# Optimization experiments

Measured on AMD Instinct MI355X. Metric: run time of the kernel, lower is better.

The kernel has to match this reference:

```python
import jax, jax.numpy as jnp
import numpy as np

B, NPG, DEG = 32, 1024, 16          # graphs, nodes/graph, avg degree
N, E = B * NPG, B * NPG * DEG        # 32768 nodes, 524288 edges
IN_C, HID, H, EDGE_D = 128, 64, 4, 8
RATIO = 0.5
K = int(np.ceil(RATIO * NPG))        # 512 nodes kept per graph (static)
SLOPE = 0.2                          # PyG GATConv LeakyReLU default


def setup_inputs() -> dict:
    key = jax.random.key(0)
    ks = jax.random.split(key, 10)
    x = jax.random.normal(ks[0], (N, IN_C), jnp.float32)
    # edges confined within each graph (block structure like PyG Batch)
    src_l = jax.random.randint(ks[1], (B, NPG * DEG), 0, NPG)
    dst_l = jax.random.randint(ks[2], (B, NPG * DEG), 0, NPG)
    off = (jnp.arange(B) * NPG)[:, None]
    edge_index = jnp.stack([(src_l + off).reshape(-1), (dst_l + off).reshape(-1)]).astype(jnp.int64)
    edge = jax.random.normal(ks[3], (E, EDGE_D), jnp.float32)
    batch_index = jnp.repeat(jnp.arange(B), NPG).astype(jnp.int64)
    s_in = 1.0 / np.sqrt(IN_C)
    W = jax.random.normal(ks[4], (IN_C, H, HID), jnp.float32) * s_in
    a_src = jax.random.normal(ks[5], (H, HID), jnp.float32) * s_in
    a_dst = jax.random.normal(ks[6], (H, HID), jnp.float32) * s_in
    b_gat = jnp.zeros((H * HID,), jnp.float32)
    W_lin = jax.random.normal(ks[7], (H * HID, HID), jnp.float32) * (1.0 / np.sqrt(H * HID))
    b_lin = jnp.zeros((HID,), jnp.float32)
    p_pool = jax.random.normal(ks[8], (HID,), jnp.float32)
    return dict(x=x, edge_index=edge_index, edge=edge, batch_index=batch_index,
                W=W, a_src=a_src, a_dst=a_dst, b_gat=b_gat,
                W_lin=W_lin, b_lin=b_lin, p_pool=p_pool)


def reference(x, edge_index, edge, batch_index, W, a_src, a_dst, b_gat, W_lin, b_lin, p_pool):
    n = x.shape[0]
    # --- GATConv (heads concat, self-loops added, softmax over incoming edges) ---
    loops = jnp.arange(n)
    src = jnp.concatenate([edge_index[0], loops])
    dst = jnp.concatenate([edge_index[1], loops])
    h = jnp.einsum('ni,ihc->nhc', x, W)                  # [N,H,C]
    al_src = (h * a_src).sum(-1)                          # [N,H]
    al_dst = (h * a_dst).sum(-1)                          # [N,H]
    e = jax.nn.leaky_relu(al_src[src] + al_dst[dst], SLOPE)  # [Etot,H]
    m = jax.ops.segment_max(e, dst, num_segments=n)
    ex = jnp.exp(e - m[dst])
    denom = jax.ops.segment_sum(ex, dst, num_segments=n)
    alpha = ex / denom[dst]                               # segment softmax per target
    out = jax.ops.segment_sum(h[src] * alpha[:, :, None], dst, num_segments=n)
    xg = out.reshape(n, H * HID) + b_gat
    # --- Linear ---
    xl = xg @ W_lin + b_lin                               # [N,HID]
    # --- TopKPooling (tanh(x.p/||p||) score, top ceil(ratio*n) per graph) ---
    score = jnp.tanh(xl @ p_pool / jnp.linalg.norm(p_pool))   # [N]
    topv, topi = jax.lax.top_k(score.reshape(B, NPG), K)      # [B,K]
    perm = (topi + (jnp.arange(B) * NPG)[:, None]).reshape(-1)  # global kept node ids
    xp = xl[perm] * topv.reshape(-1)[:, None]             # [B*K,HID], gated by score
    batch_out = jnp.repeat(jnp.arange(B), K)
    # edge filtering / remapping (padded with -1 instead of compacting)
    nmap = jnp.full((n,), -1, jnp.int32).at[perm].set(jnp.arange(B * K, dtype=jnp.int32))
    ns, nd = nmap[edge_index[0]], nmap[edge_index[1]]
    valid = (ns >= 0) & (nd >= 0)
    edge_index_new = jnp.where(valid, jnp.stack([ns, nd]), -1)
    edge_new = jnp.where(valid[:, None], edge, 0.0)
    # --- global mean/max pool (graphs are contiguous blocks of K nodes) ---
    xr = xp.reshape(B, K, HID)
    x1 = jnp.concatenate([xr.mean(axis=1), xr.max(axis=1)], axis=-1)  # [B,2*HID]
    return xp, edge_index_new, edge_new, batch_out, x1
```

## Files before the change

kernel.cpp:

```cpp
#include <hip/hip_runtime.h>
#include <math.h>

#define NN   32768
#define EE   524288
#define ETOT (EE + NN)
#define BB   32
#define NPG  1024
#define EPG  16384
#define RPG  17408
#define KK   512
#define INC  128
#define HID  64
#define NH   4
#define CC   256
#define SLOPE 0.2f

typedef __attribute__((ext_vector_type(8))) short short8;
typedef __attribute__((ext_vector_type(4))) float f32x4;

static __device__ inline unsigned short f2bf(float f) {
  unsigned u = __float_as_uint(f);
  unsigned r = (u + 0x7FFFu + ((u >> 16) & 1u)) >> 16;
  return (unsigned short)r;
}

__global__ __launch_bounds__(256) void prep_kernel(const float* __restrict__ W,
                                                   const float* __restrict__ a_src,
                                                   const float* __restrict__ a_dst,
                                                   const float* __restrict__ b_gat,
                                                   const float* __restrict__ W_lin,
                                                   const float* __restrict__ b_lin,
                                                   const float* __restrict__ p,
                                                   float* __restrict__ Mg,
                                                   float* __restrict__ cbuf,
                                                   unsigned short* __restrict__ Wt,
                                                   unsigned short* __restrict__ Wlt) {
  const int b = blockIdx.x, t = threadIdx.x;
  if (b >= 17) {
    int idx = (b - 17) * 256 + t;
    if (idx < 32768) {
      int c = idx >> 7, k = idx & 127;
      Wt[idx] = f2bf(W[k * 256 + c]);
    } else {
      int i2 = idx - 32768;
      int c = i2 >> 8, k = i2 & 255;
      Wlt[i2] = f2bf(W_lin[k * 64 + c]);
    }
    return;
  }
  __shared__ float pl[64];
  __shared__ float ql[256];
  __shared__ float red[256];
  __shared__ float red2[256];
  if (t < 64) pl[t] = p[t];
  __syncthreads();
  {
    float acc = 0.f;
    const float* wr = W_lin + t * 64;
#pragma unroll
    for (int c = 0; c < 64; c += 4) {
      float4 wv = *(const float4*)(wr + c);
      acc += wv.x * pl[c] + wv.y * pl[c + 1] + wv.z * pl[c + 2] + wv.w * pl[c + 3];
    }
    ql[t] = acc;
  }
  __syncthreads();
  if (b == 0) {
    float r = ql[t] * b_gat[t];
    if (t < 64) r += b_lin[t] * pl[t];
    red[t] = r;
    red2[t] = (t < 64) ? pl[t] * pl[t] : 0.f;
    __syncthreads();
    for (int s2 = 128; s2 > 0; s2 >>= 1) {
      if (t < s2) { red[t] += red[t + s2]; red2[t] += red2[t + s2]; }
      __syncthreads();
    }
    if (t == 0) { cbuf[0] = red[0]; cbuf[1] = 1.0f / sqrtf(red2[0]); }
    return;
  }
  if (t < 96) {
    const int i = (b - 1) * 8 + t / 12;
    const int j = t % 12;
    const int hh = j & 3;
    const float* wr = W + i * 256 + hh * 64;
    float acc = 0.f;
    if (j < 8) {
      const float* v = (j < 4 ? a_src : a_dst) + hh * 64;
#pragma unroll
      for (int c = 0; c < 64; c += 4) {
        float4 wv = *(const float4*)(wr + c);
        float4 vv = *(const float4*)(v + c);
        acc += wv.x * vv.x + wv.y * vv.y + wv.z * vv.z + wv.w * vv.w;
      }
    } else {
#pragma unroll
      for (int c = 0; c < 64; ++c) acc += wr[c] * ql[hh * 64 + c];
    }
    Mg[i * 12 + j] = acc;
  }
}

__global__ __launch_bounds__(256) void stage2_kernel(const float* __restrict__ x,
                                                     const float* __restrict__ Mg,
                                                     const unsigned short* __restrict__ Wt,
                                                     float* __restrict__ al_s,
                                                     float* __restrict__ al_d,
                                                     float* __restrict__ hq,
                                                     unsigned short* __restrict__ hbf) {
  __shared__ float smem[76 * 132];
  const int t = threadIdx.x;
  if (blockIdx.x >= 512) {
    float (*xs)[132] = (float(*)[132])smem;
    float (*MsT)[132] = (float(*)[132])(smem + 64 * 132);
    const int n0 = (blockIdx.x - 512) * 64;
    for (int r = t; r < 1536; r += 256) MsT[r % 12][r / 12] = Mg[r];
#pragma unroll
    for (int u = 0; u < 8; ++u) {
      int idx = u * 256 + t;
      int node = idx >> 5, c4 = idx & 31;
      *(float4*)(&xs[node][c4 * 4]) =
          *(const float4*)(x + (size_t)(n0 + node) * 128 + c4 * 4);
    }
    __syncthreads();
    const int node = t >> 2, q = t & 3;
    const int j0 = q * 3;
    float a0 = 0.f, a1 = 0.f, a2 = 0.f;
#pragma unroll
    for (int c4 = 0; c4 < 32; ++c4) {
      float4 xv = *(const float4*)(&xs[node][c4 * 4]);
      float4 m0 = *(const float4*)(&MsT[j0 + 0][c4 * 4]);
      float4 m1 = *(const float4*)(&MsT[j0 + 1][c4 * 4]);
      float4 m2 = *(const float4*)(&MsT[j0 + 2][c4 * 4]);
      a0 += xv.x * m0.x + xv.y * m0.y + xv.z * m0.z + xv.w * m0.w;
      a1 += xv.x * m1.x + xv.y * m1.y + xv.z * m1.z + xv.w * m1.w;
      a2 += xv.x * m2.x + xv.y * m2.y + xv.z * m2.z + xv.w * m2.w;
    }
    const int n = n0 + node;
    float vals[3] = {a0, a1, a2};
#pragma unroll
    for (int k = 0; k < 3; ++k) {
      int j = j0 + k;
      float* base = (j < 4) ? al_s : ((j < 8) ? al_d : hq);
      int jj = (j < 4) ? j : ((j < 8) ? j - 4 : j - 8);
      base[n * 4 + jj] = vals[k];
    }
    return;
  }
  const int lane = t & 63;
  const int wv = t >> 6;
  const int q = lane >> 4, nh = lane & 15;
  const int lid = blockIdx.x;
  const int node = ((lid & 7) * 64 + (lid >> 3)) * 64 + wv * 16 + nh;
  f32x4 acc[16];
#pragma unroll
  for (int mt = 0; mt < 16; ++mt) acc[mt] = (f32x4){0.f, 0.f, 0.f, 0.f};
  const float* xr = x + (size_t)node * 128;
#pragma unroll
  for (int kc = 0; kc < 4; ++kc) {
    const float* xp = xr + kc * 32 + q * 8;
    float4 v0 = *(const float4*)(xp);
    float4 v1 = *(const float4*)(xp + 4);
    short8 b;
    b[0] = (short)f2bf(v0.x); b[1] = (short)f2bf(v0.y);
    b[2] = (short)f2bf(v0.z); b[3] = (short)f2bf(v0.w);
    b[4] = (short)f2bf(v1.x); b[5] = (short)f2bf(v1.y);
    b[6] = (short)f2bf(v1.z); b[7] = (short)f2bf(v1.w);
#pragma unroll
    for (int mt = 0; mt < 16; ++mt) {
      short8 a = *(const short8*)(Wt + (size_t)(mt * 16 + nh) * 128 + kc * 32 + q * 8);
      acc[mt] = __builtin_amdgcn_mfma_f32_16x16x32_bf16(a, b, acc[mt], 0, 0, 0);
    }
  }
  unsigned short* hr = hbf + (size_t)node * 256;
#pragma unroll
  for (int mt = 0; mt < 16; ++mt) {
    ushort4 o;
    o.x = f2bf(acc[mt][0]); o.y = f2bf(acc[mt][1]);
    o.z = f2bf(acc[mt][2]); o.w = f2bf(acc[mt][3]);
    *(ushort4*)(hr + mt * 16 + q * 4) = o;
  }
}

__global__ __launch_bounds__(1024) void scan_scatter_kernel(const int* __restrict__ ei,
                                                            int* __restrict__ row_ptr,
                                                            int* __restrict__ col) {
  __shared__ int hist[NPG];
  __shared__ int lpos[NPG];
  __shared__ int wsum[16];
  const int b = blockIdx.x, t = threadIdx.x;
  const int lane = t & 63, wid = t >> 6;
  hist[t] = 0;
  __syncthreads();
  const int e0 = b * EPG;
  for (int k = t; k < EPG; k += 1024)
    atomicAdd(&hist[ei[EE + e0 + k] - b * NPG], 1);
  __syncthreads();
  const int c = hist[t] + 1;
  int inc = c;
#pragma unroll
  for (int off = 1; off < 64; off <<= 1) {
    int u = __shfl_up(inc, off, 64);
    if (lane >= off) inc += u;
  }
  if (lane == 63) wsum[wid] = inc;
  __syncthreads();
  if (wid == 0) {
    int v = (lane < 16) ? wsum[lane] : 0;
#pragma unroll
    for (int off = 1; off < 16; off <<= 1) {
      int u = __shfl_up(v, off, 64);
      if (lane >= off) v += u;
    }
    if (lane < 16) wsum[lane] = v;
  }
  __syncthreads();
  const int woff = (wid == 0) ? 0 : wsum[wid - 1];
  const int excl = woff + inc - c;
  row_ptr[b * NPG + t] = b * RPG + excl;
  lpos[t] = excl;
  if (b == 0 && t == 0) row_ptr[NN] = ETOT;
  __syncthreads();
  {
    int p0 = atomicAdd(&lpos[t], 1);
    col[b * RPG + p0] = b * NPG + t;
  }
  for (int k = t; k < EPG; k += 1024) {
    int s = ei[e0 + k];
    int d = ei[EE + e0 + k];
    int p1 = atomicAdd(&lpos[d - b * NPG], 1);
    col[b * RPG + p1] = s;
  }
}

__global__ __launch_bounds__(256) void agg_kernel(const unsigned short* __restrict__ h,
                                                  const float* __restrict__ al_s,
                                                  const float* __restrict__ al_d,
                                                  const float* __restrict__ hq,
                                                  const int* __restrict__ row_ptr,
                                                  const int* __restrict__ col,
                                                  const float* __restrict__ b_gat,
                                                  const float* __restrict__ cbuf,
                                                  unsigned short* __restrict__ outg,
                                                  float* __restrict__ score) {
  __shared__ float wsh[4][256];
  __shared__ float qsh[4][256];
  __shared__ int   osh[4][64];
  const int lane = threadIdx.x & 63;
  const int wv = threadIdx.x >> 6;
  const int hqi = lane >> 4;
  const int xcd = blockIdx.x & 7;
  const int jb = blockIdx.x >> 3;
  const int n = (xcd * 1024 + jb) * 4 + wv;
  const int beg = row_ptr[n], end = row_ptr[n + 1];
  const float4 ad4 = *(const float4*)(al_d + (size_t)n * 4);
  const char* hbase = (const char*)h + (size_t)lane * 8;
  float ax = 0.f, ay = 0.f, az = 0.f, aw = 0.f, den = 0.f, sq = 0.f;
  for (int base = beg; base < end; base += 64) {
    const int rem = end - base;
    const int cnt = rem < 64 ? rem : 64;
    if (lane < cnt) {
      const int c = col[base + lane];
      osh[wv][lane] = c << 9;
      const float4 as = *(const float4*)(al_s + (size_t)c * 4);
      float e0 = as.x + ad4.x; e0 = (e0 > 0.f) ? e0 : SLOPE * e0;
      float e1 = as.y + ad4.y; e1 = (e1 > 0.f) ? e1 : SLOPE * e1;
      float e2 = as.z + ad4.z; e2 = (e2 > 0.f) ? e2 : SLOPE * e2;
      float e3 = as.w + ad4.w; e3 = (e3 > 0.f) ? e3 : SLOPE * e3;
      *(float4*)(&wsh[wv][lane * 4]) =
          make_float4(__expf(e0), __expf(e1), __expf(e2), __expf(e3));
      *(float4*)(&qsh[wv][lane * 4]) = *(const float4*)(hq + (size_t)c * 4);
    }
    const int cm1 = cnt - 1;
    uint2 v0 = *(const uint2*)(hbase + osh[wv][0]);
    uint2 v1 = *(const uint2*)(hbase + osh[wv][1 > cm1 ? cm1 : 1]);
    uint2 v2 = *(const uint2*)(hbase + osh[wv][2 > cm1 ? cm1 : 2]);
    uint2 v3 = *(const uint2*)(hbase + osh[wv][3 > cm1 ? cm1 : 3]);
    for (int i = 0; i < cnt; ++i) {
      const float w = wsh[wv][i * 4 + hqi];
      const float hqv = qsh[wv][i * 4 + hqi];
      uint2 cur = v0; v0 = v1; v1 = v2; v2 = v3;
      int ni = i + 4; ni = ni > cm1 ? cm1 : ni;
      v3 = *(const uint2*)(hbase + osh[wv][ni]);
      den += w; sq += w * hqv;
      ax += w * __uint_as_float(cur.x << 16);
      ay += w * __uint_as_float(cur.x & 0xffff0000u);
      az += w * __uint_as_float(cur.y << 16);
      aw += w * __uint_as_float(cur.y & 0xffff0000u);
    }
  }
  const float4 bg = *(const float4*)(b_gat + lane * 4);
  ushort4 ov;
  ov.x = f2bf(ax / den + bg.x); ov.y = f2bf(ay / den + bg.y);
  ov.z = f2bf(az / den + bg.z); ov.w = f2bf(aw / den + bg.w);
  *(ushort4*)(outg + (size_t)n * 256 + lane * 4) = ov;
  float sd = sq / den;
  float s0v = __shfl(sd, 0), s1v = __shfl(sd, 16);
  float s2v = __shfl(sd, 32), s3v = __shfl(sd, 48);
  if (lane == 0)
    score[n] = tanhf((s0v + s1v + s2v + s3v + cbuf[0]) * cbuf[1]);
}

__global__ __launch_bounds__(1024) void topk_kernel(const float* __restrict__ score,
                                                    int* __restrict__ pidx_g,
                                                    float* __restrict__ tvs_g,
                                                    int* __restrict__ nmap,
                                                    float* __restrict__ out_batch) {
  __shared__ float scv[NPG];
  const int blk = blockIdx.x;
  const int b = blk >> 3, slice = blk & 7;
  const int t = threadIdx.x;
  scv[t] = score[b * NPG + t];
  __syncthreads();
  const int node = slice * 128 + (t >> 3);
  const int sub = t & 7;
  const float sc = scv[node];
  int rank = 0;
#pragma unroll
  for (int m = 0; m < 32; ++m) {
    const int j = (m * 8 + sub) * 4;
    const float4 s4 = *(const float4*)(&scv[j]);
    rank += (s4.x > sc) || (s4.x == sc && (j + 0) < node);
    rank += (s4.y > sc) || (s4.y == sc && (j + 1) < node);
    rank += (s4.z > sc) || (s4.z == sc && (j + 2) < node);
    rank += (s4.w > sc) || (s4.w == sc && (j + 3) < node);
  }
  rank += __shfl_xor(rank, 1, 64);
  rank += __shfl_xor(rank, 2, 64);
  rank += __shfl_xor(rank, 4, 64);
  if (sub == 0) {
    const int gn = b * NPG + node;
    if (rank < KK) {
      pidx_g[b * KK + rank] = node;
      tvs_g[b * KK + rank] = sc;
      nmap[gn] = b * KK + rank;
      out_batch[b * KK + rank] = (float)b;
    } else {
      nmap[gn] = -1;
    }
  }
}

__global__ __launch_bounds__(256) void gemm2xp_kernel(const unsigned short* __restrict__ outg,
                                                      const unsigned short* __restrict__ Wlt,
                                                      const float* __restrict__ bl,
                                                      const int* __restrict__ pidx_g,
                                                      const float* __restrict__ tvs_g,
                                                      float* __restrict__ out_xp,
                                                      float* __restrict__ psum,
                                                      float* __restrict__ pmax) {
  __shared__ float tile[64][68];
  __shared__ float pr[4][64];
  __shared__ float pmx[4][64];
  const int t = threadIdx.x;
  const int lane = t & 63, wv = t >> 6;
  const int q = lane >> 4, nh = lane & 15;
  const int g = blockIdx.x >> 3, o = blockIdx.x & 7;
  const int r = o * 64 + wv * 16 + nh;
  const int row = wv * 16 + nh;
  const int gnode = g * NPG + pidx_g[g * KK + r];
  const float tv = tvs_g[g * KK + r];
  f32x4 acc[4];
#pragma unroll
  for (int mt = 0; mt < 4; ++mt) acc[mt] = (f32x4){0.f, 0.f, 0.f, 0.f};
  const unsigned short* ar = outg + (size_t)gnode * 256;
#pragma unroll
  for (int kc = 0; kc < 8; ++kc) {
    short8 bf = *(const short8*)(ar + kc * 32 + q * 8);
#pragma unroll
    for (int mt = 0; mt < 4; ++mt) {
      short8 a = *(const short8*)(Wlt + (size_t)(mt * 16 + nh) * 256 + kc * 32 + q * 8);
      acc[mt] = __builtin_amdgcn_mfma_f32_16x16x32_bf16(a, bf, acc[mt], 0, 0, 0);
    }
  }
#pragma unroll
  for (int mt = 0; mt < 4; ++mt) {
    const int c4 = mt * 16 + q * 4;
    float4 bl4 = *(const float4*)(bl + c4);
    float4 o4 = make_float4((acc[mt][0] + bl4.x) * tv, (acc[mt][1] + bl4.y) * tv,
                            (acc[mt][2] + bl4.z) * tv, (acc[mt][3] + bl4.w) * tv);
    *(float4*)(out_xp + (size_t)(g * KK + r) * HID + c4) = o4;
    *(float4*)(&tile[row][c4]) = o4;
  }
  __syncthreads();
  {
    const int ch = t & 63, qr = t >> 6;
    float s = 0.f, m = -INFINITY;
#pragma unroll
    for (int rr = 0; rr < 16; ++rr) {
      float v = tile[qr * 16 + rr][ch];
      s += v; m = fmaxf(m, v);
    }
    pr[qr][ch] = s; pmx[qr][ch] = m;
  }
  __syncthreads();
  if (t < 64) {
    float s = pr[0][t] + pr[1][t] + pr[2][t] + pr[3][t];
    float m = fmaxf(fmaxf(pr[0][t], pr[1][t]), fmaxf(pr[2][t], pr[3][t]));
    m = fmaxf(fmaxf(pmx[0][t], pmx[1][t]), fmaxf(pmx[2][t], pmx[3][t]));
    psum[g * 512 + o * 64 + t] = s;
    pmax[g * 512 + o * 64 + t] = m;
  }
}

__global__ void edge_out_kernel(const int* __restrict__ ei, const float* __restrict__ edge,
                                const int* __restrict__ nmap,
                                const float* __restrict__ psum,
                                const float* __restrict__ pmax,
                                float* __restrict__ out_ei, float* __restrict__ out_edge,
                                float* __restrict__ out_x1) {
  if (blockIdx.x < BB && threadIdx.x < 64) {
    const int b = blockIdx.x, t = threadIdx.x;
    float s = 0.f, m = -INFINITY;
#pragma unroll
    for (int o = 0; o < 8; ++o) {
      s += psum[b * 512 + o * 64 + t];
      m = fmaxf(m, pmax[b * 512 + o * 64 + t]);
    }
    out_x1[b * 128 + t] = s * (1.0f / KK);
    out_x1[b * 128 + 64 + t] = m;
  }
  int e = blockIdx.x * 256 + threadIdx.x;
  if (e >= EE) return;
  int s = ei[e], d = ei[EE + e];
  int ns = nmap[s], nd = nmap[d];
  bool valid = (ns >= 0) && (nd >= 0);
  out_ei[e] = (float)(valid ? ns : -1);
  out_ei[EE + e] = (float)(valid ? nd : -1);
  const float4* ef = (const float4*)(edge + (size_t)e * 8);
  float4 z = make_float4(0.f, 0.f, 0.f, 0.f);
  float4 v0 = valid ? ef[0] : z;
  float4 v1 = valid ? ef[1] : z;
  float4* eo = (float4*)(out_edge + (size_t)e * 8);
  eo[0] = v0; eo[1] = v1;
}

extern "C" void kernel_launch(void* const* d_in, const int* in_sizes, int n_in,
                              void* d_out, int out_size, void* d_ws, size_t ws_size,
                              hipStream_t stream) {
  const float* x      = (const float*)d_in[0];
  const int*   ei     = (const int*)d_in[1];
  const float* edge   = (const float*)d_in[2];
  const float* W      = (const float*)d_in[4];
  const float* a_src  = (const float*)d_in[5];
  const float* a_dst  = (const float*)d_in[6];
  const float* b_gat  = (const float*)d_in[7];
  const float* W_lin  = (const float*)d_in[8];
  const float* b_lin  = (const float*)d_in[9];
  const float* p_pool = (const float*)d_in[10];

  char* ws = (char*)d_ws;
  size_t off = 0;
  auto alloc = [&](size_t bytes) -> void* {
    void* p = ws + off;
    off += (bytes + 255) & ~(size_t)255;
    return p;
  };
  unsigned short* hbf  = (unsigned short*)alloc((size_t)NN * CC * 2);
  unsigned short* outg = (unsigned short*)alloc((size_t)NN * CC * 2);
  float* al_s    = (float*)alloc((size_t)NN * NH * 4);
  float* al_d    = (float*)alloc((size_t)NN * NH * 4);
  float* hq      = (float*)alloc((size_t)NN * NH * 4);
  float* score   = (float*)alloc((size_t)NN * 4);
  int*   row_ptr = (int*)alloc((size_t)(NN + 1) * 4);
  int*   col     = (int*)alloc((size_t)ETOT * 4);
  int*   nmap    = (int*)alloc((size_t)NN * 4);
  int*   pidx_g  = (int*)alloc((size_t)BB * KK * 4);
  float* tvs_g   = (float*)alloc((size_t)BB * KK * 4);
  float* psum    = (float*)alloc((size_t)BB * 8 * HID * 4);
  float* pmax    = (float*)alloc((size_t)BB * 8 * HID * 4);
  unsigned short* Wt  = (unsigned short*)alloc((size_t)CC * INC * 2);
  unsigned short* Wlt = (unsigned short*)alloc((size_t)HID * CC * 2);
  float* Mg      = (float*)alloc((size_t)INC * 12 * 4);
  float* cbuf    = (float*)alloc(2 * 4);

  float* out_xp    = (float*)d_out;
  float* out_ei    = out_xp + (size_t)BB * KK * HID;
  float* out_edge  = out_ei + 2 * (size_t)EE;
  float* out_batch = out_edge + (size_t)EE * 8;
  float* out_x1    = out_batch + (size_t)BB * KK;

  prep_kernel<<<209, 256, 0, stream>>>(W, a_src, a_dst, b_gat, W_lin, b_lin,
                                       p_pool, Mg, cbuf, Wt, Wlt);
  stage2_kernel<<<1024, 256, 0, stream>>>(x, Mg, Wt, al_s, al_d, hq, hbf);
  scan_scatter_kernel<<<BB, 1024, 0, stream>>>(ei, row_ptr, col);
  agg_kernel<<<NN / 4, 256, 0, stream>>>(hbf, al_s, al_d, hq, row_ptr, col,
                                         b_gat, cbuf, outg, score);
  topk_kernel<<<256, 1024, 0, stream>>>(score, pidx_g, tvs_g, nmap, out_batch);
  gemm2xp_kernel<<<256, 256, 0, stream>>>(outg, Wlt, b_lin, pidx_g, tvs_g,
                                          out_xp, psum, pmax);
  edge_out_kernel<<<(EE + 255) / 256, 256, 0, stream>>>(ei, edge, nmap, psum, pmax,
                                                        out_ei, out_edge, out_x1);
}
```

Measured before the change: 214.5 us.

## Merge CSR build into stage2 and fuse pooling and edge output into one kernel

The CSR histogram/scan/scatter work moves into extra blocks of stage2 (now 256 threads per block, 4 nodes per thread), so it runs alongside the projection GEMM and one launch is removed. The linear-GEMM kernel and the edge-remap kernel become a single launch. The global mean/max pooling now reduces with float atomics into out_x1, which topk initialises, so the psum/pmax intermediates and their extra pass go away. The cost is atomic contention and a float sum whose order can vary, plus scan blocks that may queue behind the GEMM blocks.

```diff
diff --git a/kernel.cpp b/kernel.cpp
--- a/kernel.cpp
+++ b/kernel.cpp
@@ -22,6 +22,14 @@
   unsigned u = __float_as_uint(f);
   unsigned r = (u + 0x7FFFu + ((u >> 16) & 1u)) >> 16;
   return (unsigned short)r;
+}
+
+static __device__ inline void atomicMaxF(float* addr, float value) {
+  if (!(__float_as_uint(value) >> 31)) {
+    atomicMax((int*)addr, __float_as_int(value));
+  } else {
+    atomicMin((unsigned int*)addr, __float_as_uint(value));
+  }
 }
 
 __global__ __launch_bounds__(256) void prep_kernel(const float* __restrict__ W,
@@ -103,12 +111,62 @@
 __global__ __launch_bounds__(256) void stage2_kernel(const float* __restrict__ x,
                                                      const float* __restrict__ Mg,
                                                      const unsigned short* __restrict__ Wt,
+                                                     const int* __restrict__ ei,
                                                      float* __restrict__ al_s,
                                                      float* __restrict__ al_d,
                                                      float* __restrict__ hq,
-                                                     unsigned short* __restrict__ hbf) {
+                                                     unsigned short* __restrict__ hbf,
+                                                     int* __restrict__ row_ptr,
+                                                     int* __restrict__ col) {
   __shared__ float smem[76 * 132];
   const int t = threadIdx.x;
+  if (blockIdx.x >= 1024) {
+    int* hist = (int*)smem;
+    int* lpos = hist + NPG;
+    int* wsv  = lpos + NPG;
+    const int b = blockIdx.x - 1024;
+    const int lane = t & 63, wid = t >> 6;
+    for (int i = t; i < NPG; i += 256) hist[i] = 0;
+    __syncthreads();
+    const int e0 = b * EPG;
+    for (int k = t; k < EPG; k += 256)
+      atomicAdd(&hist[ei[EE + e0 + k] - b * NPG], 1);
+    __syncthreads();
+    const int c0 = hist[t * 4 + 0] + 1;
+    const int c1 = hist[t * 4 + 1] + 1;
+    const int c2 = hist[t * 4 + 2] + 1;
+    const int c3 = hist[t * 4 + 3] + 1;
+    const int tot = c0 + c1 + c2 + c3;
+    int inc = tot;
+#pragma unroll
+    for (int off = 1; off < 64; off <<= 1) {
+      int u = __shfl_up(inc, off, 64);
+      if (lane >= off) inc += u;
+    }
+    if (lane == 63) wsv[wid] = inc;
+    __syncthreads();
+    int woff = 0;
+    for (int w = 0; w < wid; ++w) woff += wsv[w];
+    const int p0 = woff + inc - tot;
+    const int p1 = p0 + c0, p2 = p1 + c1, p3 = p2 + c2;
+    row_ptr[b * NPG + t * 4 + 0] = b * RPG + p0; lpos[t * 4 + 0] = p0;
+    row_ptr[b * NPG + t * 4 + 1] = b * RPG + p1; lpos[t * 4 + 1] = p1;
+    row_ptr[b * NPG + t * 4 + 2] = b * RPG + p2; lpos[t * 4 + 2] = p2;
+    row_ptr[b * NPG + t * 4 + 3] = b * RPG + p3; lpos[t * 4 + 3] = p3;
+    if (b == 0 && t == 0) row_ptr[NN] = ETOT;
+    __syncthreads();
+    for (int i = t; i < NPG; i += 256) {
+      int pp = atomicAdd(&lpos[i], 1);
+      col[b * RPG + pp] = b * NPG + i;
+    }
+    for (int k = t; k < EPG; k += 256) {
+      int s = ei[e0 + k];
+      int d = ei[EE + e0 + k];
+      int pp = atomicAdd(&lpos[d - b * NPG], 1);
+      col[b * RPG + pp] = s;
+    }
+    return;
+  }
   if (blockIdx.x >= 512) {
     float (*xs)[132] = (float(*)[132])smem;
     float (*MsT)[132] = (float(*)[132])(smem + 64 * 132);
@@ -178,57 +236,6 @@
     o.x = f2bf(acc[mt][0]); o.y = f2bf(acc[mt][1]);
     o.z = f2bf(acc[mt][2]); o.w = f2bf(acc[mt][3]);
     *(ushort4*)(hr + mt * 16 + q * 4) = o;
-  }
-}
-
-__global__ __launch_bounds__(1024) void scan_scatter_kernel(const int* __restrict__ ei,
-                                                            int* __restrict__ row_ptr,
-                                                            int* __restrict__ col) {
-  __shared__ int hist[NPG];
-  __shared__ int lpos[NPG];
-  __shared__ int wsum[16];
-  const int b = blockIdx.x, t = threadIdx.x;
-  const int lane = t & 63, wid = t >> 6;
-  hist[t] = 0;
-  __syncthreads();
-  const int e0 = b * EPG;
-  for (int k = t; k < EPG; k += 1024)
-    atomicAdd(&hist[ei[EE + e0 + k] - b * NPG], 1);
-  __syncthreads();
-  const int c = hist[t] + 1;
-  int inc = c;
-#pragma unroll
-  for (int off = 1; off < 64; off <<= 1) {
-    int u = __shfl_up(inc, off, 64);
-    if (lane >= off) inc += u;
-  }
-  if (lane == 63) wsum[wid] = inc;
-  __syncthreads();
-  if (wid == 0) {
-    int v = (lane < 16) ? wsum[lane] : 0;
-#pragma unroll
-    for (int off = 1; off < 16; off <<= 1) {
-      int u = __shfl_up(v, off, 64);
-      if (lane >= off) v += u;
-    }
-    if (lane < 16) wsum[lane] = v;
-  }
-  __syncthreads();
-  const int woff = (wid == 0) ? 0 : wsum[wid - 1];
-  const int excl = woff + inc - c;
-  row_ptr[b * NPG + t] = b * RPG + excl;
-  lpos[t] = excl;
-  if (b == 0 && t == 0) row_ptr[NN] = ETOT;
-  __syncthreads();
-  {
-    int p0 = atomicAdd(&lpos[t], 1);
-    col[b * RPG + p0] = b * NPG + t;
-  }
-  for (int k = t; k < EPG; k += 1024) {
-    int s = ei[e0 + k];
-    int d = ei[EE + e0 + k];
-    int p1 = atomicAdd(&lpos[d - b * NPG], 1);
-    col[b * RPG + p1] = s;
   }
 }
 
@@ -304,11 +311,14 @@
                                                     int* __restrict__ pidx_g,
                                                     float* __restrict__ tvs_g,
                                                     int* __restrict__ nmap,
-                                                    float* __restrict__ out_batch) {
+                                                    float* __restrict__ out_batch,
+                                                    float* __restrict__ out_x1) {
   __shared__ float scv[NPG];
   const int blk = blockIdx.x;
   const int b = blk >> 3, slice = blk & 7;
   const int t = threadIdx.x;
+  if (slice == 0 && t < 128)
+    out_x1[b * 128 + t] = (t < 64) ? 0.f : -INFINITY;
   scv[t] = score[b * NPG + t];
   __syncthreads();
   const int node = slice * 128 + (t >> 3);
@@ -340,18 +350,37 @@
   }
 }
 
-__global__ __launch_bounds__(256) void gemm2xp_kernel(const unsigned short* __restrict__ outg,
-                                                      const unsigned short* __restrict__ Wlt,
-                                                      const float* __restrict__ bl,
-                                                      const int* __restrict__ pidx_g,
-                                                      const float* __restrict__ tvs_g,
-                                                      float* __restrict__ out_xp,
-                                                      float* __restrict__ psum,
-                                                      float* __restrict__ pmax) {
+__global__ __launch_bounds__(256) void final_kernel(const unsigned short* __restrict__ outg,
+                                                    const unsigned short* __restrict__ Wlt,
+                                                    const float* __restrict__ bl,
+                                                    const int* __restrict__ pidx_g,
+                                                    const float* __restrict__ tvs_g,
+                                                    const int* __restrict__ ei,
+                                                    const float* __restrict__ edge,
+                                                    const int* __restrict__ nmap,
+                                                    float* __restrict__ out_xp,
+                                                    float* __restrict__ out_ei,
+                                                    float* __restrict__ out_edge,
+                                                    float* __restrict__ out_x1) {
   __shared__ float tile[64][68];
   __shared__ float pr[4][64];
   __shared__ float pmx[4][64];
   const int t = threadIdx.x;
+  if (blockIdx.x >= 256) {
+    int e = (blockIdx.x - 256) * 256 + t;
+    int s = ei[e], d = ei[EE + e];
+    int ns = nmap[s], nd = nmap[d];
+    bool valid = (ns >= 0) && (nd >= 0);
+    out_ei[e] = (float)(valid ? ns : -1);
+    out_ei[EE + e] = (float)(valid ? nd : -1);
+    const float4* ef = (const float4*)(edge + (size_t)e * 8);
+    float4 z = make_float4(0.f, 0.f, 0.f, 0.f);
+    float4 v0 = valid ? ef[0] : z;
+    float4 v1 = valid ? ef[1] : z;
+    float4* eo = (float4*)(out_edge + (size_t)e * 8);
+    eo[0] = v0; eo[1] = v1;
+    return;
+  }
   const int lane = t & 63, wv = t >> 6;
   const int q = lane >> 4, nh = lane & 15;
   const int g = blockIdx.x >> 3, o = blockIdx.x & 7;
@@ -395,43 +424,10 @@
   __syncthreads();
   if (t < 64) {
     float s = pr[0][t] + pr[1][t] + pr[2][t] + pr[3][t];
-    float m = fmaxf(fmaxf(pr[0][t], pr[1][t]), fmaxf(pr[2][t], pr[3][t]));
-    m = fmaxf(fmaxf(pmx[0][t], pmx[1][t]), fmaxf(pmx[2][t], pmx[3][t]));
-    psum[g * 512 + o * 64 + t] = s;
-    pmax[g * 512 + o * 64 + t] = m;
-  }
-}
-
-__global__ void edge_out_kernel(const int* __restrict__ ei, const float* __restrict__ edge,
-                                const int* __restrict__ nmap,
-                                const float* __restrict__ psum,
-                                const float* __restrict__ pmax,
-                                float* __restrict__ out_ei, float* __restrict__ out_edge,
-                                float* __restrict__ out_x1) {
-  if (blockIdx.x < BB && threadIdx.x < 64) {
-    const int b = blockIdx.x, t = threadIdx.x;
-    float s = 0.f, m = -INFINITY;
-#pragma unroll
-    for (int o = 0; o < 8; ++o) {
-      s += psum[b * 512 + o * 64 + t];
-      m = fmaxf(m, pmax[b * 512 + o * 64 + t]);
-    }
-    out_x1[b * 128 + t] = s * (1.0f / KK);
-    out_x1[b * 128 + 64 + t] = m;
-  }
-  int e = blockIdx.x * 256 + threadIdx.x;
-  if (e >= EE) return;
-  int s = ei[e], d = ei[EE + e];
-  int ns = nmap[s], nd = nmap[d];
-  bool valid = (ns >= 0) && (nd >= 0);
-  out_ei[e] = (float)(valid ? ns : -1);
-  out_ei[EE + e] = (float)(valid ? nd : -1);
-  const float4* ef = (const float4*)(edge + (size_t)e * 8);
-  float4 z = make_float4(0.f, 0.f, 0.f, 0.f);
-  float4 v0 = valid ? ef[0] : z;
-  float4 v1 = valid ? ef[1] : z;
-  float4* eo = (float4*)(out_edge + (size_t)e * 8);
-  eo[0] = v0; eo[1] = v1;
+    float m = fmaxf(fmaxf(pmx[0][t], pmx[1][t]), fmaxf(pmx[2][t], pmx[3][t]));
+    atomicAdd(&out_x1[g * 128 + t], s * (1.0f / KK));
+    atomicMaxF(&out_x1[g * 128 + 64 + t], m);
+  }
 }
 
 extern "C" void kernel_launch(void* const* d_in, const int* in_sizes, int n_in,
@@ -466,8 +462,6 @@
   int*   nmap    = (int*)alloc((size_t)NN * 4);
   int*   pidx_g  = (int*)alloc((size_t)BB * KK * 4);
   float* tvs_g   = (float*)alloc((size_t)BB * KK * 4);
-  float* psum    = (float*)alloc((size_t)BB * 8 * HID * 4);
-  float* pmax    = (float*)alloc((size_t)BB * 8 * HID * 4);
   unsigned short* Wt  = (unsigned short*)alloc((size_t)CC * INC * 2);
   unsigned short* Wlt = (unsigned short*)alloc((size_t)HID * CC * 2);
   float* Mg      = (float*)alloc((size_t)INC * 12 * 4);
@@ -481,13 +475,13 @@
 
   prep_kernel<<<209, 256, 0, stream>>>(W, a_src, a_dst, b_gat, W_lin, b_lin,
                                        p_pool, Mg, cbuf, Wt, Wlt);
-  stage2_kernel<<<1024, 256, 0, stream>>>(x, Mg, Wt, al_s, al_d, hq, hbf);
-  scan_scatter_kernel<<<BB, 1024, 0, stream>>>(ei, row_ptr, col);
+  stage2_kernel<<<1056, 256, 0, stream>>>(x, Mg, Wt, ei, al_s, al_d, hq, hbf,
+                                          row_ptr, col);
   agg_kernel<<<NN / 4, 256, 0, stream>>>(hbf, al_s, al_d, hq, row_ptr, col,
                                          b_gat, cbuf, outg, score);
-  topk_kernel<<<256, 1024, 0, stream>>>(score, pidx_g, tvs_g, nmap, out_batch);
-  gemm2xp_kernel<<<256, 256, 0, stream>>>(outg, Wlt, b_lin, pidx_g, tvs_g,
-                                          out_xp, psum, pmax);
-  edge_out_kernel<<<(EE + 255) / 256, 256, 0, stream>>>(ei, edge, nmap, psum, pmax,
-                                                        out_ei, out_edge, out_x1);
-}
+  topk_kernel<<<256, 1024, 0, stream>>>(score, pidx_g, tvs_g, nmap, out_batch,
+                                        out_x1);
+  final_kernel<<<2304, 256, 0, stream>>>(outg, Wlt, b_lin, pidx_g, tvs_g,
+                                         ei, edge, nmap, out_xp, out_ei,
+                                         out_edge, out_x1);
+}
```

New measurement: 214.8 us. Within noise of the previous version (+0.1%).
